# Performance work log

Hardware: AMD Instinct MI355X
Metric: run time of the kernel (lower is better)

Reference implementation:

```python
import jax, jax.numpy as jnp
import numpy as np

B, N, D, H = 64, 4096, 128, 256


def setup_inputs() -> dict:
    key = jax.random.key(0)
    k1, k2, k3 = jax.random.split(key, 3)
    feats = jax.random.normal(k1, (B, N, D), dtype=jnp.float32)
    # Linear init scale ~ 1/sqrt(fan_in) to keep scores well-conditioned
    W1 = jax.random.normal(k2, (D, H), dtype=jnp.float32) / np.sqrt(D)
    b1 = jnp.zeros((H,), dtype=jnp.float32)
    W2 = jax.random.normal(k3, (H, 1), dtype=jnp.float32) / np.sqrt(H)
    b2 = jnp.zeros((1,), dtype=jnp.float32)
    return {"feats": feats, "W1": W1, "b1": b1, "W2": W2, "b2": b2}


def reference(feats, W1, b1, W2, b2):
    # scalar attention score per node: fc = Linear -> ReLU -> Linear(->1)
    h = jax.nn.relu(jnp.einsum('bnd,dh->bnh', feats, W1) + b1)  # [B,N,H]
    scores = jnp.einsum('bnh,ho->bno', h, W2) + b2              # [B,N,1]
    w = jax.nn.softmax(scores, axis=1)                          # softmax over nodes
    out = jnp.sum(w * feats, axis=1)                            # [B,D]
    return out
```

## Files before the change

### kernel.cpp

```cpp
#include <hip/hip_runtime.h>
#include <math.h>

#define BB 64
#define NN 4096
#define DD 128
#define HH 256
#define MB 256
#define NBLK (BB * NN / MB)
#define PSTRIDE 132

typedef __attribute__((ext_vector_type(8))) _Float16 f16x8;
typedef __attribute__((ext_vector_type(4))) float f32x4;

static __device__ __forceinline__ void gload_lds16(const void* g, void* l) {
    __builtin_amdgcn_global_load_lds(
        (const __attribute__((address_space(1))) unsigned int*)g,
        (__attribute__((address_space(3))) unsigned int*)l, 16, 0, 0);
}

__global__ __launch_bounds__(256) void k_prep(const float* __restrict__ W1,
                                              char* __restrict__ Bws) {
    const int k = blockIdx.x;
    const int c = threadIdx.x;
    const _Float16 h = (_Float16)W1[k * HH + c];
    const int chunk = c >> 4, cl = c & 15;
    const int off = ((cl << 8) + (k << 1)) ^ ((cl & 7) << 4);
    *(_Float16*)(Bws + chunk * 4096 + off) = h;
}

__global__ __launch_bounds__(256, 2) void k_fused(const float* __restrict__ feats,
                                                  const char* __restrict__ Bws,
                                                  const float* __restrict__ b1,
                                                  const float* __restrict__ W2,
                                                  float* __restrict__ parts) {
    __shared__ char  Bl[65536];
    __shared__ float scores_l[256];
    __shared__ float ew[256];
    __shared__ float wacc[4][128];
    __shared__ float redm[4], redz[4];

    const int tid  = threadIdx.x;
    const int lane = tid & 63;
    const int wv   = tid >> 6;
    const int blk  = blockIdx.x;
    const int rl   = lane & 15;
    const int q    = lane >> 4;

    #pragma unroll
    for (int it = 0; it < 16; ++it)
        gload_lds16(Bws + it * 4096 + tid * 16, Bl + it * 4096 + tid * 16);

    f16x8 af[4][4];
    const float* fbase = feats + (size_t)blk * MB * DD;
    #pragma unroll
    for (int t = 0; t < 4; ++t) {
        const float* rp = fbase + (wv * 64 + t * 16 + rl) * DD + q * 8;
        #pragma unroll
        for (int kk = 0; kk < 4; ++kk) {
            float4 v0 = *(const float4*)(rp + kk * 32);
            float4 v1 = *(const float4*)(rp + kk * 32 + 4);
            f16x8 a;
            a[0] = (_Float16)v0.x; a[1] = (_Float16)v0.y;
            a[2] = (_Float16)v0.z; a[3] = (_Float16)v0.w;
            a[4] = (_Float16)v1.x; a[5] = (_Float16)v1.y;
            a[6] = (_Float16)v1.z; a[7] = (_Float16)v1.w;
            af[t][kk] = a;
        }
    }
    __syncthreads();

    float sp[4][4] = {{0,0,0,0},{0,0,0,0},{0,0,0,0},{0,0,0,0}};
    const int brow = rl << 8;
    const int bswz = (rl & 7) << 4;
    const int bq   = q << 4;

    for (int chunk = 0; chunk < 16; ++chunk) {
        const float bbv = b1[chunk * 16 + rl];
        const float ww  = W2[chunk * 16 + rl];
        const char* cb = Bl + chunk * 4096;
        f32x4 acc0 = {0,0,0,0}, acc1 = {0,0,0,0}, acc2 = {0,0,0,0}, acc3 = {0,0,0,0};
        #pragma unroll
        for (int kk = 0; kk < 4; ++kk) {
            f16x8 bf = *(const f16x8*)(cb + (((brow + (kk << 6) + bq)) ^ bswz));
            acc0 = __builtin_amdgcn_mfma_f32_16x16x32_f16(af[0][kk], bf, acc0, 0, 0, 0);
            acc1 = __builtin_amdgcn_mfma_f32_16x16x32_f16(af[1][kk], bf, acc1, 0, 0, 0);
            acc2 = __builtin_amdgcn_mfma_f32_16x16x32_f16(af[2][kk], bf, acc2, 0, 0, 0);
            acc3 = __builtin_amdgcn_mfma_f32_16x16x32_f16(af[3][kk], bf, acc3, 0, 0, 0);
        }
        #pragma unroll
        for (int j = 0; j < 4; ++j) {
            sp[0][j] += fmaxf(acc0[j] + bbv, 0.f) * ww;
            sp[1][j] += fmaxf(acc1[j] + bbv, 0.f) * ww;
            sp[2][j] += fmaxf(acc2[j] + bbv, 0.f) * ww;
            sp[3][j] += fmaxf(acc3[j] + bbv, 0.f) * ww;
        }
    }

    #pragma unroll
    for (int m = 1; m < 16; m <<= 1)
        #pragma unroll
        for (int t = 0; t < 4; ++t)
            #pragma unroll
            for (int j = 0; j < 4; ++j)
                sp[t][j] += __shfl_xor(sp[t][j], m);
    if (rl == 0) {
        #pragma unroll
        for (int t = 0; t < 4; ++t)
            #pragma unroll
            for (int j = 0; j < 4; ++j)
                scores_l[wv * 64 + t * 16 + q * 4 + j] = sp[t][j];
    }
    __syncthreads();

    const float s = scores_l[tid];
    float mx = s;
    #pragma unroll
    for (int o = 1; o < 64; o <<= 1) mx = fmaxf(mx, __shfl_xor(mx, o));
    if (lane == 0) redm[wv] = mx;
    __syncthreads();
    mx = fmaxf(fmaxf(redm[0], redm[1]), fmaxf(redm[2], redm[3]));
    const float e = expf(s - mx);
    ew[tid] = e;
    float z = e;
    #pragma unroll
    for (int o = 1; o < 64; o <<= 1) z += __shfl_xor(z, o);
    if (lane == 0) redz[wv] = z;
    __syncthreads();
    const float zblk = redz[0] + redz[1] + redz[2] + redz[3];

    const float w0 = ew[wv * 64 +  0 + rl];
    const float w1 = ew[wv * 64 + 16 + rl];
    const float w2 = ew[wv * 64 + 32 + rl];
    const float w3 = ew[wv * 64 + 48 + rl];
    float acc[4][8];
    #pragma unroll
    for (int kk = 0; kk < 4; ++kk)
        #pragma unroll
        for (int e8 = 0; e8 < 8; ++e8)
            acc[kk][e8] = w0 * (float)af[0][kk][e8] + w1 * (float)af[1][kk][e8]
                        + w2 * (float)af[2][kk][e8] + w3 * (float)af[3][kk][e8];
    #pragma unroll
    for (int m = 1; m < 16; m <<= 1)
        #pragma unroll
        for (int kk = 0; kk < 4; ++kk)
            #pragma unroll
            for (int e8 = 0; e8 < 8; ++e8)
                acc[kk][e8] += __shfl_xor(acc[kk][e8], m);
    if (rl == 0) {
        #pragma unroll
        for (int kk = 0; kk < 4; ++kk)
            #pragma unroll
            for (int e8 = 0; e8 < 8; ++e8)
                wacc[wv][kk * 32 + q * 8 + e8] = acc[kk][e8];
    }
    __syncthreads();

    if (tid < 128) {
        float p = wacc[0][tid] + wacc[1][tid] + wacc[2][tid] + wacc[3][tid];
        parts[blk * PSTRIDE + tid] = p;
    } else if (tid == 128) {
        parts[blk * PSTRIDE + 128] = mx;
        parts[blk * PSTRIDE + 129] = zblk;
    }
}

__global__ __launch_bounds__(128) void k_out(const float* __restrict__ parts,
                                             float* __restrict__ out) {
    const int b = blockIdx.x;
    const int d = threadIdx.x;
    const float* pb = parts + (size_t)b * 16 * PSTRIDE;
    float M = -1e30f;
    #pragma unroll
    for (int i = 0; i < 16; ++i) M = fmaxf(M, pb[i * PSTRIDE + 128]);
    float num = 0.f, den = 0.f;
    #pragma unroll
    for (int i = 0; i < 16; ++i) {
        const float sc = expf(pb[i * PSTRIDE + 128] - M);
        num = fmaf(sc, pb[i * PSTRIDE + d], num);
        den = fmaf(sc, pb[i * PSTRIDE + 129], den);
    }
    out[b * DD + d] = num / den;
}

extern "C" void kernel_launch(void* const* d_in, const int* in_sizes, int n_in,
                              void* d_out, int out_size, void* d_ws, size_t ws_size,
                              hipStream_t stream) {
    const float* feats = (const float*)d_in[0];
    const float* W1    = (const float*)d_in[1];
    const float* b1    = (const float*)d_in[2];
    const float* W2    = (const float*)d_in[3];
    float* out = (float*)d_out;

    char*  Bws   = (char*)d_ws;
    float* parts = (float*)((char*)d_ws + 65536);

    hipLaunchKernelGGL(k_prep, dim3(DD), dim3(HH), 0, stream, W1, Bws);
    hipLaunchKernelGGL(k_fused, dim3(NBLK), dim3(256), 0, stream,
                       feats, Bws, b1, W2, parts);
    hipLaunchKernelGGL(k_out, dim3(BB), dim3(128), 0, stream, parts, out);
}
```

Measured before the change: 54.45 us.

## Read W1 fragments directly from global memory with register double-buffering, drop LDS staging

Removes the 64KB LDS copy of the fp16 W1 and has each lane load its B fragments straight from a plain transposed global layout (cache-resident), double-buffered in registers across the H-chunk loop. Dropping the LDS allocation and the block barrier allows up to 4 blocks per CU (launch bounds raised) instead of LDS-limited occupancy. The cost is repeated L2/L1 traffic for W1 per wave and higher register pressure from the fully unrolled chunk loop with two B buffers, which could cause spills under the tighter 4-block register budget.

```diff
diff --git a/kernel.cpp b/kernel.cpp
--- a/kernel.cpp
+++ b/kernel.cpp
@@ -12,28 +12,18 @@
 typedef __attribute__((ext_vector_type(8))) _Float16 f16x8;
 typedef __attribute__((ext_vector_type(4))) float f32x4;
 
-static __device__ __forceinline__ void gload_lds16(const void* g, void* l) {
-    __builtin_amdgcn_global_load_lds(
-        (const __attribute__((address_space(1))) unsigned int*)g,
-        (__attribute__((address_space(3))) unsigned int*)l, 16, 0, 0);
+__global__ __launch_bounds__(256) void k_prep(const float* __restrict__ W1,
+                                              _Float16* __restrict__ Bws) {
+    const int k = blockIdx.x;
+    const int c = threadIdx.x;
+    Bws[c * DD + k] = (_Float16)W1[k * HH + c];
 }
 
-__global__ __launch_bounds__(256) void k_prep(const float* __restrict__ W1,
-                                              char* __restrict__ Bws) {
-    const int k = blockIdx.x;
-    const int c = threadIdx.x;
-    const _Float16 h = (_Float16)W1[k * HH + c];
-    const int chunk = c >> 4, cl = c & 15;
-    const int off = ((cl << 8) + (k << 1)) ^ ((cl & 7) << 4);
-    *(_Float16*)(Bws + chunk * 4096 + off) = h;
-}
-
-__global__ __launch_bounds__(256, 2) void k_fused(const float* __restrict__ feats,
-                                                  const char* __restrict__ Bws,
+__global__ __launch_bounds__(256, 4) void k_fused(const float* __restrict__ feats,
+                                                  const _Float16* __restrict__ Bws,
                                                   const float* __restrict__ b1,
                                                   const float* __restrict__ W2,
                                                   float* __restrict__ parts) {
-    __shared__ char  Bl[65536];
     __shared__ float scores_l[256];
     __shared__ float ew[256];
     __shared__ float wacc[4][128];
@@ -45,10 +35,6 @@
     const int blk  = blockIdx.x;
     const int rl   = lane & 15;
     const int q    = lane >> 4;
-
-    #pragma unroll
-    for (int it = 0; it < 16; ++it)
-        gload_lds16(Bws + it * 4096 + tid * 16, Bl + it * 4096 + tid * 16);
 
     f16x8 af[4][4];
     const float* fbase = feats + (size_t)blk * MB * DD;
@@ -67,26 +53,36 @@
             af[t][kk] = a;
         }
     }
-    __syncthreads();
+
+    const _Float16* bbase = Bws + rl * DD + q * 8;
 
     float sp[4][4] = {{0,0,0,0},{0,0,0,0},{0,0,0,0},{0,0,0,0}};
-    const int brow = rl << 8;
-    const int bswz = (rl & 7) << 4;
-    const int bq   = q << 4;
 
+    f16x8 bb[2][4];
+    #pragma unroll
+    for (int kk = 0; kk < 4; ++kk)
+        bb[0][kk] = *(const f16x8*)(bbase + kk * 32);
+
+    #pragma unroll
     for (int chunk = 0; chunk < 16; ++chunk) {
-        const float bbv = b1[chunk * 16 + rl];
-        const float ww  = W2[chunk * 16 + rl];
-        const char* cb = Bl + chunk * 4096;
+        const int cur = chunk & 1;
+        if (chunk < 15) {
+            const _Float16* nb = bbase + (chunk + 1) * 16 * DD;
+            #pragma unroll
+            for (int kk = 0; kk < 4; ++kk)
+                bb[cur ^ 1][kk] = *(const f16x8*)(nb + kk * 32);
+        }
         f32x4 acc0 = {0,0,0,0}, acc1 = {0,0,0,0}, acc2 = {0,0,0,0}, acc3 = {0,0,0,0};
         #pragma unroll
         for (int kk = 0; kk < 4; ++kk) {
-            f16x8 bf = *(const f16x8*)(cb + (((brow + (kk << 6) + bq)) ^ bswz));
+            const f16x8 bf = bb[cur][kk];
             acc0 = __builtin_amdgcn_mfma_f32_16x16x32_f16(af[0][kk], bf, acc0, 0, 0, 0);
             acc1 = __builtin_amdgcn_mfma_f32_16x16x32_f16(af[1][kk], bf, acc1, 0, 0, 0);
             acc2 = __builtin_amdgcn_mfma_f32_16x16x32_f16(af[2][kk], bf, acc2, 0, 0, 0);
             acc3 = __builtin_amdgcn_mfma_f32_16x16x32_f16(af[3][kk], bf, acc3, 0, 0, 0);
         }
+        const float bbv = b1[chunk * 16 + rl];
+        const float ww  = W2[chunk * 16 + rl];
         #pragma unroll
         for (int j = 0; j < 4; ++j) {
             sp[0][j] += fmaxf(acc0[j] + bbv, 0.f) * ww;
@@ -191,8 +187,8 @@
     const float* W2    = (const float*)d_in[3];
     float* out = (float*)d_out;
 
-    char*  Bws   = (char*)d_ws;
-    float* parts = (float*)((char*)d_ws + 65536);
+    _Float16* Bws  = (_Float16*)d_ws;
+    float*   parts = (float*)((char*)d_ws + 65536);
 
     hipLaunchKernelGGL(k_prep, dim3(DD), dim3(HH), 0, stream, W1, Bws);
     hipLaunchKernelGGL(k_fused, dim3(NBLK), dim3(256), 0, stream,
```

Measured after the change: 212.9 us. 3.91x slower.

## Halve LDS weight buffer by loading W1 in two halves

Applied to the files above, without the earlier changes.

Shrinks the shared-memory buffer for the fp16 W1 tile to half size. The first half of the hidden chunks is computed, then the second half is reloaded into the same buffer between two barriers. This lowers per-block LDS so more blocks can be resident per CU. The cost is an extra mid-kernel barrier and a second global-to-LDS load phase that cannot overlap compute.

```diff
diff --git a/kernel.cpp b/kernel.cpp
--- a/kernel.cpp
+++ b/kernel.cpp
@@ -7,6 +7,7 @@
 #define HH 256
 #define MB 256
 #define NBLK (BB * NN / MB)
+#define PPB 16
 #define PSTRIDE 132
 
 typedef __attribute__((ext_vector_type(8))) _Float16 f16x8;
@@ -33,7 +34,7 @@
                                                   const float* __restrict__ b1,
                                                   const float* __restrict__ W2,
                                                   float* __restrict__ parts) {
-    __shared__ char  Bl[65536];
+    __shared__ char  Bl[32768];
     __shared__ float scores_l[256];
     __shared__ float ew[256];
     __shared__ float wacc[4][128];
@@ -47,7 +48,7 @@
     const int q    = lane >> 4;
 
     #pragma unroll
-    for (int it = 0; it < 16; ++it)
+    for (int it = 0; it < 8; ++it)
         gload_lds16(Bws + it * 4096 + tid * 16, Bl + it * 4096 + tid * 16);
 
     f16x8 af[4][4];
@@ -74,27 +75,41 @@
     const int bswz = (rl & 7) << 4;
     const int bq   = q << 4;
 
-    for (int chunk = 0; chunk < 16; ++chunk) {
-        const float bbv = b1[chunk * 16 + rl];
-        const float ww  = W2[chunk * 16 + rl];
-        const char* cb = Bl + chunk * 4096;
-        f32x4 acc0 = {0,0,0,0}, acc1 = {0,0,0,0}, acc2 = {0,0,0,0}, acc3 = {0,0,0,0};
-        #pragma unroll
-        for (int kk = 0; kk < 4; ++kk) {
-            f16x8 bf = *(const f16x8*)(cb + (((brow + (kk << 6) + bq)) ^ bswz));
-            acc0 = __builtin_amdgcn_mfma_f32_16x16x32_f16(af[0][kk], bf, acc0, 0, 0, 0);
-            acc1 = __builtin_amdgcn_mfma_f32_16x16x32_f16(af[1][kk], bf, acc1, 0, 0, 0);
-            acc2 = __builtin_amdgcn_mfma_f32_16x16x32_f16(af[2][kk], bf, acc2, 0, 0, 0);
-            acc3 = __builtin_amdgcn_mfma_f32_16x16x32_f16(af[3][kk], bf, acc3, 0, 0, 0);
-        }
-        #pragma unroll
-        for (int j = 0; j < 4; ++j) {
-            sp[0][j] += fmaxf(acc0[j] + bbv, 0.f) * ww;
-            sp[1][j] += fmaxf(acc1[j] + bbv, 0.f) * ww;
-            sp[2][j] += fmaxf(acc2[j] + bbv, 0.f) * ww;
-            sp[3][j] += fmaxf(acc3[j] + bbv, 0.f) * ww;
-        }
-    }
+#define CHUNK_COMPUTE(CHUNK)                                                       \
+    do {                                                                           \
+        const float bbv = b1[(CHUNK) * 16 + rl];                                   \
+        const float ww  = W2[(CHUNK) * 16 + rl];                                   \
+        const char* cb = Bl + ((CHUNK) & 7) * 4096;                                \
+        f32x4 acc0 = {0,0,0,0}, acc1 = {0,0,0,0}, acc2 = {0,0,0,0}, acc3 = {0,0,0,0};\
+        _Pragma("unroll")                                                          \
+        for (int kk = 0; kk < 4; ++kk) {                                           \
+            f16x8 bf = *(const f16x8*)(cb + (((brow + (kk << 6) + bq)) ^ bswz));   \
+            acc0 = __builtin_amdgcn_mfma_f32_16x16x32_f16(af[0][kk], bf, acc0, 0,0,0);\
+            acc1 = __builtin_amdgcn_mfma_f32_16x16x32_f16(af[1][kk], bf, acc1, 0,0,0);\
+            acc2 = __builtin_amdgcn_mfma_f32_16x16x32_f16(af[2][kk], bf, acc2, 0,0,0);\
+            acc3 = __builtin_amdgcn_mfma_f32_16x16x32_f16(af[3][kk], bf, acc3, 0,0,0);\
+        }                                                                          \
+        _Pragma("unroll")                                                          \
+        for (int j = 0; j < 4; ++j) {                                              \
+            sp[0][j] += fmaxf(acc0[j] + bbv, 0.f) * ww;                            \
+            sp[1][j] += fmaxf(acc1[j] + bbv, 0.f) * ww;                            \
+            sp[2][j] += fmaxf(acc2[j] + bbv, 0.f) * ww;                            \
+            sp[3][j] += fmaxf(acc3[j] + bbv, 0.f) * ww;                            \
+        }                                                                          \
+    } while (0)
+
+    #pragma unroll
+    for (int chunk = 0; chunk < 8; ++chunk) CHUNK_COMPUTE(chunk);
+
+    __syncthreads();
+    #pragma unroll
+    for (int it = 0; it < 8; ++it)
+        gload_lds16(Bws + 32768 + it * 4096 + tid * 16, Bl + it * 4096 + tid * 16);
+    __syncthreads();
+
+    #pragma unroll
+    for (int chunk = 8; chunk < 16; ++chunk) CHUNK_COMPUTE(chunk);
+#undef CHUNK_COMPUTE
 
     #pragma unroll
     for (int m = 1; m < 16; m <<= 1)
@@ -168,13 +183,13 @@
                                              float* __restrict__ out) {
     const int b = blockIdx.x;
     const int d = threadIdx.x;
-    const float* pb = parts + (size_t)b * 16 * PSTRIDE;
+    const float* pb = parts + (size_t)b * PPB * PSTRIDE;
     float M = -1e30f;
     #pragma unroll
-    for (int i = 0; i < 16; ++i) M = fmaxf(M, pb[i * PSTRIDE + 128]);
+    for (int i = 0; i < PPB; ++i) M = fmaxf(M, pb[i * PSTRIDE + 128]);
     float num = 0.f, den = 0.f;
     #pragma unroll
-    for (int i = 0; i < 16; ++i) {
+    for (int i = 0; i < PPB; ++i) {
         const float sc = expf(pb[i * PSTRIDE + 128] - M);
         num = fmaf(sc, pb[i * PSTRIDE + d], num);
         den = fmaf(sc, pb[i * PSTRIDE + 129], den);
```

Result: slower. 68.58 us (+25.9%).

## Split each block's rows across eight waves to raise occupancy

Applied to the files above, without the earlier changes.

Doubles threads per block to 512 so each wave handles 32 rows instead of 64, halving per-thread fragment and accumulator registers while sharing the same LDS copy of W1. The intent is more resident waves per CU to hide global load latency on the feats stream. The softmax reduction duplicates scores across the two halves of the block and corrects the sum by halving it; the chunk loop is also fully unrolled. Risks are more reduction and synchronisation overhead and more waves contending for MFMA units.

```diff
diff --git a/kernel.cpp b/kernel.cpp
--- a/kernel.cpp
+++ b/kernel.cpp
@@ -6,7 +6,9 @@
 #define DD 128
 #define HH 256
 #define MB 256
+#define NTHR 512
 #define NBLK (BB * NN / MB)
+#define PPB 16
 #define PSTRIDE 132
 
 typedef __attribute__((ext_vector_type(8))) _Float16 f16x8;
@@ -28,16 +30,16 @@
     *(_Float16*)(Bws + chunk * 4096 + off) = h;
 }
 
-__global__ __launch_bounds__(256, 2) void k_fused(const float* __restrict__ feats,
-                                                  const char* __restrict__ Bws,
-                                                  const float* __restrict__ b1,
-                                                  const float* __restrict__ W2,
-                                                  float* __restrict__ parts) {
+__global__ __launch_bounds__(NTHR, 4) void k_fused(const float* __restrict__ feats,
+                                                   const char* __restrict__ Bws,
+                                                   const float* __restrict__ b1,
+                                                   const float* __restrict__ W2,
+                                                   float* __restrict__ parts) {
     __shared__ char  Bl[65536];
     __shared__ float scores_l[256];
     __shared__ float ew[256];
-    __shared__ float wacc[4][128];
-    __shared__ float redm[4], redz[4];
+    __shared__ float wacc[8][128];
+    __shared__ float redm[8], redz[8];
 
     const int tid  = threadIdx.x;
     const int lane = tid & 63;
@@ -47,14 +49,14 @@
     const int q    = lane >> 4;
 
     #pragma unroll
-    for (int it = 0; it < 16; ++it)
-        gload_lds16(Bws + it * 4096 + tid * 16, Bl + it * 4096 + tid * 16);
-
-    f16x8 af[4][4];
+    for (int it = 0; it < 8; ++it)
+        gload_lds16(Bws + it * 8192 + tid * 16, Bl + it * 8192 + tid * 16);
+
+    f16x8 af[2][4];
     const float* fbase = feats + (size_t)blk * MB * DD;
     #pragma unroll
-    for (int t = 0; t < 4; ++t) {
-        const float* rp = fbase + (wv * 64 + t * 16 + rl) * DD + q * 8;
+    for (int t = 0; t < 2; ++t) {
+        const float* rp = fbase + (wv * 32 + t * 16 + rl) * DD + q * 8;
         #pragma unroll
         for (int kk = 0; kk < 4; ++kk) {
             float4 v0 = *(const float4*)(rp + kk * 32);
@@ -69,76 +71,72 @@
     }
     __syncthreads();
 
-    float sp[4][4] = {{0,0,0,0},{0,0,0,0},{0,0,0,0},{0,0,0,0}};
+    float sp[2][4] = {{0,0,0,0},{0,0,0,0}};
     const int brow = rl << 8;
     const int bswz = (rl & 7) << 4;
     const int bq   = q << 4;
 
+    #pragma unroll
     for (int chunk = 0; chunk < 16; ++chunk) {
         const float bbv = b1[chunk * 16 + rl];
         const float ww  = W2[chunk * 16 + rl];
         const char* cb = Bl + chunk * 4096;
-        f32x4 acc0 = {0,0,0,0}, acc1 = {0,0,0,0}, acc2 = {0,0,0,0}, acc3 = {0,0,0,0};
+        f32x4 acc0 = {0,0,0,0}, acc1 = {0,0,0,0};
         #pragma unroll
         for (int kk = 0; kk < 4; ++kk) {
             f16x8 bf = *(const f16x8*)(cb + (((brow + (kk << 6) + bq)) ^ bswz));
             acc0 = __builtin_amdgcn_mfma_f32_16x16x32_f16(af[0][kk], bf, acc0, 0, 0, 0);
             acc1 = __builtin_amdgcn_mfma_f32_16x16x32_f16(af[1][kk], bf, acc1, 0, 0, 0);
-            acc2 = __builtin_amdgcn_mfma_f32_16x16x32_f16(af[2][kk], bf, acc2, 0, 0, 0);
-            acc3 = __builtin_amdgcn_mfma_f32_16x16x32_f16(af[3][kk], bf, acc3, 0, 0, 0);
         }
         #pragma unroll
         for (int j = 0; j < 4; ++j) {
             sp[0][j] += fmaxf(acc0[j] + bbv, 0.f) * ww;
             sp[1][j] += fmaxf(acc1[j] + bbv, 0.f) * ww;
-            sp[2][j] += fmaxf(acc2[j] + bbv, 0.f) * ww;
-            sp[3][j] += fmaxf(acc3[j] + bbv, 0.f) * ww;
         }
     }
 
     #pragma unroll
     for (int m = 1; m < 16; m <<= 1)
         #pragma unroll
-        for (int t = 0; t < 4; ++t)
+        for (int t = 0; t < 2; ++t)
             #pragma unroll
             for (int j = 0; j < 4; ++j)
                 sp[t][j] += __shfl_xor(sp[t][j], m);
     if (rl == 0) {
         #pragma unroll
-        for (int t = 0; t < 4; ++t)
+        for (int t = 0; t < 2; ++t)
             #pragma unroll
             for (int j = 0; j < 4; ++j)
-                scores_l[wv * 64 + t * 16 + q * 4 + j] = sp[t][j];
-    }
-    __syncthreads();
-
-    const float s = scores_l[tid];
+                scores_l[wv * 32 + t * 16 + q * 4 + j] = sp[t][j];
+    }
+    __syncthreads();
+
+    const float s = scores_l[tid & 255];
     float mx = s;
     #pragma unroll
     for (int o = 1; o < 64; o <<= 1) mx = fmaxf(mx, __shfl_xor(mx, o));
     if (lane == 0) redm[wv] = mx;
     __syncthreads();
-    mx = fmaxf(fmaxf(redm[0], redm[1]), fmaxf(redm[2], redm[3]));
+    mx = fmaxf(fmaxf(fmaxf(redm[0], redm[1]), fmaxf(redm[2], redm[3])),
+               fmaxf(fmaxf(redm[4], redm[5]), fmaxf(redm[6], redm[7])));
     const float e = expf(s - mx);
-    ew[tid] = e;
+    if (tid < 256) ew[tid] = e;
     float z = e;
     #pragma unroll
     for (int o = 1; o < 64; o <<= 1) z += __shfl_xor(z, o);
     if (lane == 0) redz[wv] = z;
     __syncthreads();
-    const float zblk = redz[0] + redz[1] + redz[2] + redz[3];
-
-    const float w0 = ew[wv * 64 +  0 + rl];
-    const float w1 = ew[wv * 64 + 16 + rl];
-    const float w2 = ew[wv * 64 + 32 + rl];
-    const float w3 = ew[wv * 64 + 48 + rl];
+    const float zblk = 0.5f * (redz[0] + redz[1] + redz[2] + redz[3] +
+                               redz[4] + redz[5] + redz[6] + redz[7]);
+
+    const float w0 = ew[wv * 32 +  0 + rl];
+    const float w1 = ew[wv * 32 + 16 + rl];
     float acc[4][8];
     #pragma unroll
     for (int kk = 0; kk < 4; ++kk)
         #pragma unroll
         for (int e8 = 0; e8 < 8; ++e8)
-            acc[kk][e8] = w0 * (float)af[0][kk][e8] + w1 * (float)af[1][kk][e8]
-                        + w2 * (float)af[2][kk][e8] + w3 * (float)af[3][kk][e8];
+            acc[kk][e8] = w0 * (float)af[0][kk][e8] + w1 * (float)af[1][kk][e8];
     #pragma unroll
     for (int m = 1; m < 16; m <<= 1)
         #pragma unroll
@@ -156,7 +154,8 @@
     __syncthreads();
 
     if (tid < 128) {
-        float p = wacc[0][tid] + wacc[1][tid] + wacc[2][tid] + wacc[3][tid];
+        float p = wacc[0][tid] + wacc[1][tid] + wacc[2][tid] + wacc[3][tid]
+                + wacc[4][tid] + wacc[5][tid] + wacc[6][tid] + wacc[7][tid];
         parts[blk * PSTRIDE + tid] = p;
     } else if (tid == 128) {
         parts[blk * PSTRIDE + 128] = mx;
@@ -168,13 +167,13 @@
                                              float* __restrict__ out) {
     const int b = blockIdx.x;
     const int d = threadIdx.x;
-    const float* pb = parts + (size_t)b * 16 * PSTRIDE;
+    const float* pb = parts + (size_t)b * PPB * PSTRIDE;
     float M = -1e30f;
     #pragma unroll
-    for (int i = 0; i < 16; ++i) M = fmaxf(M, pb[i * PSTRIDE + 128]);
+    for (int i = 0; i < PPB; ++i) M = fmaxf(M, pb[i * PSTRIDE + 128]);
     float num = 0.f, den = 0.f;
     #pragma unroll
-    for (int i = 0; i < 16; ++i) {
+    for (int i = 0; i < PPB; ++i) {
         const float sc = expf(pb[i * PSTRIDE + 128] - M);
         num = fmaf(sc, pb[i * PSTRIDE + d], num);
         den = fmaf(sc, pb[i * PSTRIDE + 129], den);
@@ -195,7 +194,7 @@
     float* parts = (float*)((char*)d_ws + 65536);
 
     hipLaunchKernelGGL(k_prep, dim3(DD), dim3(HH), 0, stream, W1, Bws);
-    hipLaunchKernelGGL(k_fused, dim3(NBLK), dim3(256), 0, stream,
+    hipLaunchKernelGGL(k_fused, dim3(NBLK), dim3(NTHR), 0, stream,
                        feats, Bws, b1, W2, parts);
     hipLaunchKernelGGL(k_out, dim3(BB), dim3(128), 0, stream, parts, out);
 }
```

After: 77.49 us. 1.42x slower.
